# Kernel tuning notes

Measured on AMD Instinct MI355X. Metric: run time of the kernel, lower is better.

## Reference

```python
import jax, jax.numpy as jnp
import numpy as np

B, A, NBH, F, G, H = 8, 512, 64, 128, 50, 8
DH = F // H
CUTOFF = 5.0


def setup_inputs() -> dict:
    key = jax.random.key(0)
    ks = jax.random.split(key, 13)
    x = jax.random.normal(ks[0], (B, A, F), jnp.float32)
    e = jax.random.normal(ks[1], (B, A, F), jnp.float32)
    t = jax.random.normal(ks[2], (B, F), jnp.float32)
    # distances in [0, 1.2*cutoff] so some pairs fall outside the cutoff
    r_ij = jax.random.uniform(ks[3], (B, A, NBH), jnp.float32) * (1.2 * CUTOFF)
    f_ij = jax.random.normal(ks[4], (B, A, NBH, G), jnp.float32)
    neighbors = jax.random.randint(ks[5], (B, A, NBH), 0, A, jnp.int32)
    neighbor_mask = jax.random.randint(ks[6], (B, A, NBH), 0, 2, jnp.int32).astype(bool)
    sF = 1.0 / np.sqrt(F).astype(np.float32)
    W_filt = jax.random.normal(ks[7], (G, F), jnp.float32) * (1.0 / np.sqrt(G).astype(np.float32))
    b_filt = jnp.zeros((F,), jnp.float32)
    Wq = jax.random.normal(ks[8], (F, F), jnp.float32) * sF
    Wk = jax.random.normal(ks[9], (F, F), jnp.float32) * sF
    Wv = jax.random.normal(ks[10], (F, F), jnp.float32) * sF
    Wo = jax.random.normal(ks[11], (F, F), jnp.float32) * sF
    bo = jnp.zeros((F,), jnp.float32)
    return dict(e=e, x=x, t=t, r_ij=r_ij, f_ij=f_ij,
                W_filt=W_filt, b_filt=b_filt, Wq=Wq, Wk=Wk, Wv=Wv, Wo=Wo, bo=bo,
                neighbors=neighbors, neighbor_mask=neighbor_mask)


def reference(e, x, t, r_ij, f_ij, W_filt, b_filt, Wq, Wk, Wv, Wo, bo,
              neighbors, neighbor_mask):
    # ---- filter network + cosine cutoff: W (B, A, NBH, F) ----
    W = f_ij @ W_filt + b_filt
    C = 0.5 * (jnp.cos(jnp.pi * r_ij / CUTOFF) + 1.0)
    C = C * (r_ij < CUTOFF).astype(x.dtype)           # (B, A, NBH)
    W = W * C[..., None]

    # ---- neighbor gather: nbh (B, A, NBH, F) ----
    bidx = jnp.arange(B)[:, None, None]
    nbh = x[bidx, neighbors]                           # irregular gather
    nbh = nbh * W                                      # filter-modulated messages

    # ---- EgoAttention: central atom queries its neighbors ----
    q = (x @ Wq).reshape(B, A, H, DH)                  # bahd
    k = (nbh @ Wk).reshape(B, A, NBH, H, DH)           # banhd
    v = (nbh @ Wv).reshape(B, A, NBH, H, DH)
    scale = np.float32(1.0 / np.sqrt(DH))
    scores = jnp.einsum('bahd,banhd->bahn', q, k) * scale
    scores = jnp.where(neighbor_mask[:, :, None, :], scores, jnp.float32(-1e9))
    attn = jax.nn.softmax(scores, axis=-1)             # over neighbors
    msg = jnp.einsum('bahn,banhd->bahd', attn, v).reshape(B, A, F)
    v_out = msg @ Wo + bo

    # ---- residual (apply_transition_function=False branch) ----
    return x + v_out
```

## Files before the change

### kernel.cpp

```cpp
#include <hip/hip_runtime.h>
#include <math.h>

#define BB 8
#define AA 512
#define NBH 64
#define FF 128
#define GG 50
#define CUTOFF 5.0f

typedef __attribute__((ext_vector_type(8)))  short bf16x8;
typedef __attribute__((ext_vector_type(4)))  float f32x4;
typedef __attribute__((ext_vector_type(16))) float f32x16;

#define WKV_ELEMS (4*8*64*8)
#define WQO_ELEMS (8*4*64*8)
#define WF_ELEMS  (4*4*64*8)
#define XB_ELEMS  (BB*AA*FF)

__device__ __forceinline__ short f2bf(float f) {
    union { float f; unsigned u; } v; v.f = f;
    unsigned r = v.u + 0x7fffu + ((v.u >> 16) & 1u);
    return (short)(r >> 16);
}
__device__ __forceinline__ short f2bf_fast(float f) {
    return (short)((__float_as_uint(f) + 0x8000u) >> 16);
}
__device__ __forceinline__ unsigned int pk2bf(float a, float b) {
    unsigned int ua = __float_as_uint(a) + 0x8000u;
    unsigned int ub = __float_as_uint(b) + 0x8000u;
    return __builtin_amdgcn_perm(ub, ua, 0x07060302u);
}
__device__ __forceinline__ bf16x8 ld_f8_bfpk(const float* p) {
    const float2* p2 = (const float2*)p;
    float2 a = p2[0], b = p2[1], c = p2[2], d = p2[3];
    union { unsigned int u[4]; bf16x8 v; } r;
    r.u[0] = pk2bf(a.x, a.y);
    r.u[1] = pk2bf(b.x, b.y);
    r.u[2] = pk2bf(c.x, c.y);
    r.u[3] = pk2bf(d.x, d.y);
    return r.v;
}

__device__ __forceinline__ float row16_sum(float x) {
    int t;
    t = __builtin_amdgcn_update_dpp(0, __float_as_int(x), 0x128, 0xf, 0xf, true); x += __int_as_float(t);
    t = __builtin_amdgcn_update_dpp(0, __float_as_int(x), 0x124, 0xf, 0xf, true); x += __int_as_float(t);
    t = __builtin_amdgcn_update_dpp(0, __float_as_int(x), 0x122, 0xf, 0xf, true); x += __int_as_float(t);
    t = __builtin_amdgcn_update_dpp(0, __float_as_int(x), 0x121, 0xf, 0xf, true); x += __int_as_float(t);
    return x;
}

__global__ void prep_kernel(const float* __restrict__ Wk,
                            const float* __restrict__ Wv,
                            const float* __restrict__ Wq,
                            const float* __restrict__ Wo,
                            const float* __restrict__ Wf,
                            const float* __restrict__ b_filt,
                            const float* __restrict__ x,
                            short* __restrict__ ws)
{
    int gid = blockIdx.x * blockDim.x + threadIdx.x;
    if (gid < 2 * WKV_ELEMS) {
        const float* src = (gid < WKV_ELEMS) ? Wk : Wv;
        int idx = gid & (WKV_ELEMS - 1);
        int j = idx & 7, l = (idx >> 3) & 63, rest = idx >> 9;
        int s = rest & 7, w = rest >> 3;
        int k = 16 * s + ((l >> 5) << 3) + j;
        int n = 32 * w + (l & 31);
        ws[gid] = f2bf(src[k * FF + n]);
    } else if (gid < 2 * WKV_ELEMS + 2 * WQO_ELEMS) {
        int idx2 = gid - 2 * WKV_ELEMS;
        const float* src = (idx2 < WQO_ELEMS) ? Wq : Wo;
        int idx = idx2 & (WQO_ELEMS - 1);
        int j = idx & 7, l = (idx >> 3) & 63, rest = idx >> 9;
        int s = rest & 3, c = rest >> 2;
        int k = 32 * s + (l >> 4) * 8 + j;
        int n = 16 * c + (l & 15);
        ws[gid] = f2bf(src[k * FF + n]);
    } else if (gid < 2 * WKV_ELEMS + 2 * WQO_ELEMS + WF_ELEMS) {
        int idx = gid - 2 * WKV_ELEMS - 2 * WQO_ELEMS;
        int j = idx & 7, l = (idx >> 3) & 63, rest = idx >> 9;
        int s = rest & 3, w = rest >> 2;
        int k = 16 * s + ((l >> 5) << 3) + j;
        int n = 32 * w + (l & 31);
        float v = (k < GG) ? Wf[k * FF + n] : (k == GG ? b_filt[n] : 0.0f);
        ws[gid] = f2bf(v);
    } else {
        int idx = gid - 2 * WKV_ELEMS - 2 * WQO_ELEMS - WF_ELEMS;
        ws[gid] = f2bf(x[idx]);
    }
}

__global__ __launch_bounds__(256, 4)
void tdt_main(const float* __restrict__ x,
              const float* __restrict__ r_ij,
              const float* __restrict__ f_ij,
              const float* __restrict__ bo,
              const int*   __restrict__ neighbors,
              const int*   __restrict__ nmask,
              const short* __restrict__ WkB,
              const short* __restrict__ WvB,
              const short* __restrict__ WqB,
              const short* __restrict__ WoB,
              const short* __restrict__ WfB,
              const short* __restrict__ xB,
              float* __restrict__ out)
{
    const int ba   = blockIdx.x;
    const int b    = ba >> 9;
    const int tid  = threadIdx.x;
    const int lane = tid & 63;
    const int w    = tid >> 6;
    const int l15  = lane & 15;
    const int quad = lane >> 4;
    const int l31  = lane & 31;
    const int khalf = (lane >> 5) << 3;
    const int w5_4  = (lane >> 5) * 4;

    __shared__ short X_s[NBH * FF];
    __shared__ short msg_bf[FF];
    __shared__ float C_s[NBH];

    const float* xrow = x + (size_t)ba * FF;
    const unsigned short* xbu = (const unsigned short*)xB + (size_t)b * AA * FF;
    const size_t bao = (size_t)ba;

    {
#pragma unroll
        for (int j = 0; j < 4; ++j) {
            int row = 16 * w + 4 * j + (lane >> 4);
            int nbn = neighbors[bao * NBH + row];
            int kk  = (lane & 15) ^ (row & 7);
            const unsigned short* src = xbu + (size_t)nbn * FF + (size_t)(kk * 8);
            __builtin_amdgcn_global_load_lds(
                (const __attribute__((address_space(1))) void*)src,
                (__attribute__((address_space(3))) void*)&X_s[(16 * w + 4 * j) * FF],
                16, 0, 0);
        }
    }

    if (w == 0) {
        float r = r_ij[bao * NBH + lane];
        float c = 0.5f * (__cosf((float)M_PI * r * (1.0f / CUTOFF)) + 1.0f);
        C_s[lane] = (r < CUTOFF) ? c : 0.0f;
    }
    unsigned long long mask64 = __ballot(nmask[bao * NBH + lane] != 0);

    float qvm;
    {
        const short* xbrow = &xB[(size_t)ba * FF];
        bf16x8 xa[4];
#pragma unroll
        for (int s = 0; s < 4; ++s)
            xa[s] = *(const bf16x8*)&xbrow[32 * s + quad * 8];
        float qv0, qv1;
#pragma unroll
        for (int ct = 0; ct < 2; ++ct) {
            int cg = 2 * w + ct;
            f32x4 z = {0.f, 0.f, 0.f, 0.f};
#pragma unroll
            for (int s = 0; s < 4; ++s) {
                bf16x8 bq = *(const bf16x8*)&WqB[((cg * 4 + s) * 64 + lane) * 8];
                z = __builtin_amdgcn_mfma_f32_16x16x32_bf16(xa[s], bq, z, 0, 0, 0);
            }
            if (ct == 0) qv0 = z[0]; else qv1 = z[0];
        }
        qvm = (((lane >> 4) & 1) ? qv1 : qv0) * 0.25f;
    }
    __syncthreads();

    {
        const float* fm0 = f_ij + bao * (size_t)(NBH * GG) + (size_t)l31 * GG;
        const int c_hi = 4 * w + (l31 >> 3);
        const int c_lo = l31 & 7;
#pragma unroll
        for (int mt = 0; mt < 2; ++mt) {
            f32x16 wacc;
#pragma unroll
            for (int r = 0; r < 16; ++r) wacc[r] = 0.0f;
            const float* fm = fm0 + mt * 32 * GG;
#pragma unroll
            for (int s = 0; s < 4; ++s) {
                bf16x8 bfw = *(const bf16x8*)&WfB[((w * 4 + s) * 64 + lane) * 8];
                bf16x8 fa;
                if (s < 3) {
                    fa = ld_f8_bfpk(fm + 16 * s + khalf);
                } else {
#pragma unroll
                    for (int jj = 0; jj < 8; ++jj) fa[jj] = 0;
                    if (lane < 32) {
                        fa[0] = f2bf_fast(fm[48]);
                        fa[1] = f2bf_fast(fm[49]);
                        fa[2] = (short)0x3F80;
                    }
                }
                wacc = __builtin_amdgcn_mfma_f32_32x32x16_bf16(fa, bfw, wacc, 0, 0, 0);
            }
#pragma unroll
            for (int r = 0; r < 16; ++r) {
                int   n   = 32 * mt + (r & 3) + 8 * (r >> 2) + w5_4;
                float cn  = C_s[n];
                int   a   = n * FF + (((c_hi ^ (n & 7)) << 3) | c_lo);
                float xv  = __uint_as_float((unsigned)((const unsigned short*)X_s)[a] << 16);
                X_s[a] = f2bf_fast(wacc[r] * cn * xv);
            }
        }
    }
    __syncthreads();

    float sum = 0.0f, acc = 0.0f;
#pragma unroll
    for (int mt = 0; mt < 2; ++mt) {
        int m = 32 * mt + l31;
        f32x16 kacc, vacc;
#pragma unroll
        for (int r = 0; r < 16; ++r) { kacc[r] = 0.0f; vacc[r] = 0.0f; }
#pragma unroll
        for (int s = 0; s < 8; ++s) {
            bf16x8 ma = *(const bf16x8*)&X_s[m * FF + (((2 * s + (lane >> 5)) ^ (m & 7)) << 3)];
            bf16x8 bk = *(const bf16x8*)&WkB[((w * 8 + s) * 64 + lane) * 8];
            bf16x8 bv = *(const bf16x8*)&WvB[((w * 8 + s) * 64 + lane) * 8];
            kacc = __builtin_amdgcn_mfma_f32_32x32x16_bf16(ma, bk, kacc, 0, 0, 0);
            vacc = __builtin_amdgcn_mfma_f32_32x32x16_bf16(ma, bv, vacc, 0, 0, 0);
        }
#pragma unroll
        for (int r = 0; r < 16; ++r) {
            float sr = row16_sum(kacc[r] * qvm);
            int   n  = 32 * mt + (r & 3) + 8 * (r >> 2) + w5_4;
            float e  = ((mask64 >> n) & 1ull) ? __expf(sr) : 0.0f;
            sum += e;
            acc  = fmaf(e, vacc[r], acc);
        }
    }
    sum += __shfl_xor(sum, 32, 64);
    acc += __shfl_xor(acc, 32, 64);
    if (lane < 32) msg_bf[32 * w + l31] = f2bf_fast(acc / sum);
    __syncthreads();

    {
        bf16x8 mga[4];
#pragma unroll
        for (int s = 0; s < 4; ++s)
            mga[s] = *(const bf16x8*)&msg_bf[s * 32 + quad * 8];
#pragma unroll
        for (int ct = 0; ct < 2; ++ct) {
            int cg = 2 * w + ct;
            f32x4 z = {0.f, 0.f, 0.f, 0.f};
#pragma unroll
            for (int s = 0; s < 4; ++s) {
                bf16x8 bw = *(const bf16x8*)&WoB[((cg * 4 + s) * 64 + lane) * 8];
                z = __builtin_amdgcn_mfma_f32_16x16x32_bf16(mga[s], bw, z, 0, 0, 0);
            }
            if (quad == 0) {
                int col = cg * 16 + l15;
                out[bao * FF + col] = z[0] + xrow[col] + bo[col];
            }
        }
    }
}

extern "C" void kernel_launch(void* const* d_in, const int* in_sizes, int n_in,
                              void* d_out, int out_size, void* d_ws, size_t ws_size,
                              hipStream_t stream) {
    const float* x      = (const float*)d_in[1];
    const float* r_ij   = (const float*)d_in[3];
    const float* f_ij   = (const float*)d_in[4];
    const float* W_filt = (const float*)d_in[5];
    const float* b_filt = (const float*)d_in[6];
    const float* Wq     = (const float*)d_in[7];
    const float* Wk     = (const float*)d_in[8];
    const float* Wv     = (const float*)d_in[9];
    const float* Wo     = (const float*)d_in[10];
    const float* bo     = (const float*)d_in[11];
    const int*   nbr    = (const int*)d_in[12];
    const int*   msk    = (const int*)d_in[13];
    float* out = (float*)d_out;

    short* ws  = (short*)d_ws;
    short* WkB = ws;
    short* WvB = ws + WKV_ELEMS;
    short* WqB = ws + 2 * WKV_ELEMS;
    short* WoB = ws + 2 * WKV_ELEMS + WQO_ELEMS;
    short* WfB = ws + 2 * WKV_ELEMS + 2 * WQO_ELEMS;
    short* xB  = ws + 2 * WKV_ELEMS + 2 * WQO_ELEMS + WF_ELEMS;

    int prep_total = 2 * WKV_ELEMS + 2 * WQO_ELEMS + WF_ELEMS + XB_ELEMS;
    hipLaunchKernelGGL(prep_kernel, dim3(prep_total / 256), dim3(256), 0, stream,
                       Wk, Wv, Wq, Wo, W_filt, b_filt, x, ws);
    hipLaunchKernelGGL(tdt_main, dim3(BB * AA), dim3(256), 0, stream,
                       x, r_ij, f_ij, bo, nbr, msk,
                       WkB, WvB, WqB, WoB, WfB, xB, out);
}
```

Measured before the change: 160.2 us.

## Switch K/V projection to 16x16x32 MFMA tiles with per-head column groups

Restructures the key/value projection and attention accumulation from 32x32x16 MFMA tiles to 16x16x32 tiles over four 16-row neighbor blocks and two 16-column groups per wave, so each column group maps to one head. The Wk/Wv weight pre-layout is changed to match the Wq/Wo packing. The goal is lower accumulator register pressure and no per-lane head selection for q, which should help occupancy. In exchange it issues more, smaller MFMAs, reloads the weight fragments per row block, and adds extra cross-lane shuffle reductions.

Result: faster. 152.7 us (-4.6%).

```diff
diff --git a/kernel.cpp b/kernel.cpp
--- a/kernel.cpp
+++ b/kernel.cpp
@@ -60,21 +60,14 @@
                             short* __restrict__ ws)
 {
     int gid = blockIdx.x * blockDim.x + threadIdx.x;
-    if (gid < 2 * WKV_ELEMS) {
-        const float* src = (gid < WKV_ELEMS) ? Wk : Wv;
+    if (gid < 2 * WKV_ELEMS + 2 * WQO_ELEMS) {
+        const float* src = (gid < WKV_ELEMS) ? Wk :
+                           (gid < 2 * WKV_ELEMS) ? Wv :
+                           (gid < 2 * WKV_ELEMS + WQO_ELEMS) ? Wq : Wo;
         int idx = gid & (WKV_ELEMS - 1);
         int j = idx & 7, l = (idx >> 3) & 63, rest = idx >> 9;
-        int s = rest & 7, w = rest >> 3;
-        int k = 16 * s + ((l >> 5) << 3) + j;
-        int n = 32 * w + (l & 31);
-        ws[gid] = f2bf(src[k * FF + n]);
-    } else if (gid < 2 * WKV_ELEMS + 2 * WQO_ELEMS) {
-        int idx2 = gid - 2 * WKV_ELEMS;
-        const float* src = (idx2 < WQO_ELEMS) ? Wq : Wo;
-        int idx = idx2 & (WQO_ELEMS - 1);
-        int j = idx & 7, l = (idx >> 3) & 63, rest = idx >> 9;
         int s = rest & 3, c = rest >> 2;
-        int k = 32 * s + (l >> 4) * 8 + j;
+        int k = 32 * s + ((l >> 4) << 3) + j;
         int n = 16 * c + (l & 15);
         ws[gid] = f2bf(src[k * FF + n]);
     } else if (gid < 2 * WKV_ELEMS + 2 * WQO_ELEMS + WF_ELEMS) {
@@ -146,14 +139,13 @@
     }
     unsigned long long mask64 = __ballot(nmask[bao * NBH + lane] != 0);
 
-    float qvm;
+    float qs[2];
     {
         const short* xbrow = &xB[(size_t)ba * FF];
         bf16x8 xa[4];
 #pragma unroll
         for (int s = 0; s < 4; ++s)
             xa[s] = *(const bf16x8*)&xbrow[32 * s + quad * 8];
-        float qv0, qv1;
 #pragma unroll
         for (int ct = 0; ct < 2; ++ct) {
             int cg = 2 * w + ct;
@@ -163,9 +155,8 @@
                 bf16x8 bq = *(const bf16x8*)&WqB[((cg * 4 + s) * 64 + lane) * 8];
                 z = __builtin_amdgcn_mfma_f32_16x16x32_bf16(xa[s], bq, z, 0, 0, 0);
             }
-            if (ct == 0) qv0 = z[0]; else qv1 = z[0];
-        }
-        qvm = (((lane >> 4) & 1) ? qv1 : qv0) * 0.25f;
+            qs[ct] = z[0] * 0.25f;
+        }
     }
     __syncthreads();
 
@@ -208,33 +199,54 @@
     }
     __syncthreads();
 
-    float sum = 0.0f, acc = 0.0f;
-#pragma unroll
-    for (int mt = 0; mt < 2; ++mt) {
-        int m = 32 * mt + l31;
-        f32x16 kacc, vacc;
-#pragma unroll
-        for (int r = 0; r < 16; ++r) { kacc[r] = 0.0f; vacc[r] = 0.0f; }
-#pragma unroll
-        for (int s = 0; s < 8; ++s) {
-            bf16x8 ma = *(const bf16x8*)&X_s[m * FF + (((2 * s + (lane >> 5)) ^ (m & 7)) << 3)];
-            bf16x8 bk = *(const bf16x8*)&WkB[((w * 8 + s) * 64 + lane) * 8];
-            bf16x8 bv = *(const bf16x8*)&WvB[((w * 8 + s) * 64 + lane) * 8];
-            kacc = __builtin_amdgcn_mfma_f32_32x32x16_bf16(ma, bk, kacc, 0, 0, 0);
-            vacc = __builtin_amdgcn_mfma_f32_32x32x16_bf16(ma, bv, vacc, 0, 0, 0);
-        }
-#pragma unroll
-        for (int r = 0; r < 16; ++r) {
-            float sr = row16_sum(kacc[r] * qvm);
-            int   n  = 32 * mt + (r & 3) + 8 * (r >> 2) + w5_4;
-            float e  = ((mask64 >> n) & 1ull) ? __expf(sr) : 0.0f;
-            sum += e;
-            acc  = fmaf(e, vacc[r], acc);
-        }
-    }
-    sum += __shfl_xor(sum, 32, 64);
-    acc += __shfl_xor(acc, 32, 64);
-    if (lane < 32) msg_bf[32 * w + l31] = f2bf_fast(acc / sum);
+    float sums[2] = {0.0f, 0.0f}, accs[2] = {0.0f, 0.0f};
+#pragma unroll
+    for (int mtl = 0; mtl < 4; ++mtl) {
+        bf16x8 A[4];
+#pragma unroll
+        for (int s = 0; s < 4; ++s) {
+            int row = 16 * mtl + l15;
+            int chunk = (4 * s + quad) ^ (row & 7);
+            A[s] = *(const bf16x8*)&X_s[row * FF + chunk * 8];
+        }
+#pragma unroll
+        for (int ct = 0; ct < 2; ++ct) {
+            int cg = 2 * w + ct;
+            f32x4 kacc = {0.f, 0.f, 0.f, 0.f};
+#pragma unroll
+            for (int s = 0; s < 4; ++s) {
+                bf16x8 bk = *(const bf16x8*)&WkB[((cg * 4 + s) * 64 + lane) * 8];
+                kacc = __builtin_amdgcn_mfma_f32_16x16x32_bf16(A[s], bk, kacc, 0, 0, 0);
+            }
+            float e[4];
+#pragma unroll
+            for (int r = 0; r < 4; ++r) {
+                float sr = row16_sum(kacc[r] * qs[ct]);
+                int   n  = 16 * mtl + quad * 4 + r;
+                e[r] = ((mask64 >> n) & 1ull) ? __expf(sr) : 0.0f;
+                sums[ct] += e[r];
+            }
+            f32x4 vacc = {0.f, 0.f, 0.f, 0.f};
+#pragma unroll
+            for (int s = 0; s < 4; ++s) {
+                bf16x8 bv = *(const bf16x8*)&WvB[((cg * 4 + s) * 64 + lane) * 8];
+                vacc = __builtin_amdgcn_mfma_f32_16x16x32_bf16(A[s], bv, vacc, 0, 0, 0);
+            }
+#pragma unroll
+            for (int r = 0; r < 4; ++r) accs[ct] = fmaf(e[r], vacc[r], accs[ct]);
+        }
+    }
+#pragma unroll
+    for (int ct = 0; ct < 2; ++ct) {
+        sums[ct] += __shfl_xor(sums[ct], 16, 64);
+        sums[ct] += __shfl_xor(sums[ct], 32, 64);
+        accs[ct] += __shfl_xor(accs[ct], 16, 64);
+        accs[ct] += __shfl_xor(accs[ct], 32, 64);
+    }
+    if (quad == 0) {
+        msg_bf[16 * (2 * w + 0) + l15] = f2bf_fast(accs[0] / sums[0]);
+        msg_bf[16 * (2 * w + 1) + l15] = f2bf_fast(accs[1] / sums[1]);
+    }
     __syncthreads();
 
     {
```
